# Kernel tuning notes

Measured on AMD Instinct MI355X. Metric: run time of the kernel, lower is better.

The kernel has to match this reference:

```python
import jax, jax.numpy as jnp
import numpy as np

B, N, D = 16, 2048, 64

def setup_inputs() -> dict:
    key = jax.random.key(0)
    kq, kk, kv = jax.random.split(key, 3)
    queries = jax.random.normal(kq, (B, N, D), dtype=jnp.float32)
    keys = jax.random.normal(kk, (B, N, D), dtype=jnp.float32)
    values = jax.random.normal(kv, (B, N, D), dtype=jnp.float32)
    scaling_factor = jnp.asarray(np.sqrt(D), dtype=jnp.float32)
    return {"queries": queries, "keys": keys, "values": values, "scaling_factor": scaling_factor}

def reference(queries, keys, values, scaling_factor):
    # scores: [B, N, N] = Q K^T / scale
    scores = jnp.einsum('bqd,bkd->bqk', queries, keys) / scaling_factor
    atn = jax.nn.softmax(scores, axis=2)
    return jnp.einsum('bqk,bkd->bqd', atn, values)
```

## Files before the change

kernel.cpp:

```cpp
#include <hip/hip_runtime.h>
#include <hip/hip_bf16.h>

#define BATCH 16
#define SEQ 2048
#define DIM 64

typedef __attribute__((ext_vector_type(8))) __bf16 bf16x8;
typedef __attribute__((ext_vector_type(8))) unsigned short u16x8;
typedef __attribute__((ext_vector_type(4))) unsigned int u32x4;
typedef __attribute__((ext_vector_type(16))) float f32x16;

#if __has_builtin(__builtin_amdgcn_exp2f)
#define EXP2F(x) __builtin_amdgcn_exp2f(x)
#else
#define EXP2F(x) __expf(0.69314718055994531f * (x))
#endif

__device__ __forceinline__ unsigned short f2bf_hw(float f) {
    __bf16 h = (__bf16)f;
    return __builtin_bit_cast(unsigned short, h);
}

__device__ __forceinline__ unsigned int pk_bf16(float lo, float hi) {
    unsigned int a = f2bf_hw(lo), b = f2bf_hw(hi);
    return a | (b << 16);
}

__device__ __forceinline__ bf16x8 ld_bf8_g(const unsigned short* p) {
    u16x8 u = *(const u16x8*)p;
    return __builtin_bit_cast(bf16x8, u);
}

__global__ __launch_bounds__(256)
void preconvert_kv(const float* __restrict__ K, const float* __restrict__ V,
                   unsigned short* __restrict__ Ks, unsigned short* __restrict__ Vts) {
    const int tid = threadIdx.x;
    if (blockIdx.x < 256) {
        const int b = blockIdx.x >> 4;
        const int t = blockIdx.x & 15;
        const float* src = K + ((size_t)(b * SEQ + t * 128)) * DIM;
        unsigned short* dst = Ks + ((size_t)(b * 16 + t)) * 8192;
        #pragma unroll
        for (int p = 0; p < 4; ++p) {
            const int cid = p * 256 + tid;
            const int key = cid >> 3, g = cid & 7;
            const int d0 = (g >> 1) * 16 + (g & 1) * 8;
            float4 x0 = *(const float4*)(src + key * DIM + d0);
            float4 x1 = *(const float4*)(src + key * DIM + d0 + 4);
            u16x8 o;
            o[0] = f2bf_hw(x0.x); o[1] = f2bf_hw(x0.y); o[2] = f2bf_hw(x0.z); o[3] = f2bf_hw(x0.w);
            o[4] = f2bf_hw(x1.x); o[5] = f2bf_hw(x1.y); o[6] = f2bf_hw(x1.z); o[7] = f2bf_hw(x1.w);
            *(u16x8*)(dst + (g * 128 + key) * 8) = o;
        }
    } else {
        const int vb = blockIdx.x - 256;
        const int b = vb >> 4;
        const int t = vb & 15;
        const float* src = V + ((size_t)(b * SEQ + t * 128)) * DIM;
        unsigned short* dst = Vts + ((size_t)(b * 16 + t)) * 8192;
        #pragma unroll
        for (int p = 0; p < 4; ++p) {
            const int cid = p * 256 + tid;
            const int g = cid >> 6, d = cid & 63;
            const int k0 = (g >> 1) * 16 + (g & 1) * 8;
            u16x8 o;
            #pragma unroll
            for (int j = 0; j < 8; ++j) o[j] = f2bf_hw(src[(k0 + j) * DIM + d]);
            *(u16x8*)(dst + (g * 64 + d) * 8) = o;
        }
    }
}

__global__ __launch_bounds__(256, 2)
void attn_flash_kernel(const float* __restrict__ Q,
                       const unsigned short* __restrict__ Ks,
                       const unsigned short* __restrict__ Vts,
                       const float* __restrict__ scaling,
                       float* __restrict__ O) {
    __shared__ float comb[3 * 64 * 66];

    const int tid  = threadIdx.x;
    const int w    = tid >> 6;
    const int lane = tid & 63;
    const int m    = lane & 31;
    const int h    = lane >> 5;

    const int x  = blockIdx.x;
    const int b  = ((x & 7) << 1) | ((x >> 3) & 1);
    const int q0 = (x >> 4) * 64;

    const float csc = 1.4426950408889634f / scaling[0];

    bf16x8 aq0[4], aq1[4];
    #pragma unroll
    for (int s = 0; s < 2; ++s) {
        const float* qsrc = Q + ((size_t)(b * SEQ + q0 + s * 32 + m)) * DIM + h * 8;
        #pragma unroll
        for (int c = 0; c < 4; ++c) {
            float4 x0 = *(const float4*)(qsrc + c * 16);
            float4 x1 = *(const float4*)(qsrc + c * 16 + 4);
            u32x4 pk;
            pk[0] = pk_bf16(x0.x * csc, x0.y * csc);
            pk[1] = pk_bf16(x0.z * csc, x0.w * csc);
            pk[2] = pk_bf16(x1.x * csc, x1.y * csc);
            pk[3] = pk_bf16(x1.z * csc, x1.w * csc);
            (s ? aq1 : aq0)[c] = __builtin_bit_cast(bf16x8, pk);
        }
    }

    f32x16 Oacc0[2], Oacc1[2];
    #pragma unroll
    for (int dt = 0; dt < 2; ++dt)
        #pragma unroll
        for (int r = 0; r < 16; ++r) { Oacc0[dt][r] = 0.f; Oacc1[dt][r] = 0.f; }
    float psum0 = 0.f, psum1 = 0.f;

    const unsigned short* Kbase = Ks + ((size_t)(b * 16 + w * 4)) * 8192;
    const unsigned short* Vbase = Vts + ((size_t)(b * 16 + w * 4)) * 8192;

    bf16x8 kc[4], bv[2][2];
    #pragma unroll
    for (int c = 0; c < 4; ++c)
        kc[c] = ld_bf8_g(&Kbase[((c * 2 + h) * 128 + m) * 8]);
    #pragma unroll
    for (int c2 = 0; c2 < 2; ++c2)
        #pragma unroll
        for (int dt = 0; dt < 2; ++dt)
            bv[c2][dt] = ld_bf8_g(&Vbase[((c2 * 2 + h) * 64 + dt * 32 + m) * 8]);

    #pragma unroll 1
    for (int st = 0; st < 16; ++st) {
        f32x16 S0, S1;
        #pragma unroll
        for (int r = 0; r < 16; ++r) { S0[r] = 0.f; S1[r] = 0.f; }
        #pragma unroll
        for (int c = 0; c < 4; ++c) {
            S0 = __builtin_amdgcn_mfma_f32_32x32x16_bf16(kc[c], aq0[c], S0, 0, 0, 0);
            S1 = __builtin_amdgcn_mfma_f32_32x32x16_bf16(kc[c], aq1[c], S1, 0, 0, 0);
        }

        const int stn = (st < 15) ? st + 1 : 15;
        const unsigned short* Ktn = Kbase + (size_t)(stn >> 2) * 8192;
        const unsigned short* Vtn = Vbase + (size_t)(stn >> 2) * 8192;
        const int tn = stn & 3;
        bf16x8 kn[4], vn[2][2];
        #pragma unroll
        for (int c = 0; c < 4; ++c)
            kn[c] = ld_bf8_g(&Ktn[((c * 2 + h) * 128 + tn * 32 + m) * 8]);
        #pragma unroll
        for (int c2 = 0; c2 < 2; ++c2)
            #pragma unroll
            for (int dt = 0; dt < 2; ++dt)
                vn[c2][dt] = ld_bf8_g(&Vtn[(((2 * tn + c2) * 2 + h) * 64 + dt * 32 + m) * 8]);

        unsigned int d0a[8], d0b[8], dsa[8], dsb[8];
        #pragma unroll
        for (int k = 0; k < 4; ++k) {
            float a0 = EXP2F(S0[4 * k + 0]), a1 = EXP2F(S0[4 * k + 1]);
            float a2 = EXP2F(S0[4 * k + 2]), a3 = EXP2F(S0[4 * k + 3]);
            psum0 += (a0 + a1) + (a2 + a3);
            d0a[2 * k + 0] = pk_bf16(a0, a1);
            d0a[2 * k + 1] = pk_bf16(a2, a3);
            float b0 = EXP2F(S1[4 * k + 0]), b1 = EXP2F(S1[4 * k + 1]);
            float b2 = EXP2F(S1[4 * k + 2]), b3 = EXP2F(S1[4 * k + 3]);
            psum1 += (b0 + b1) + (b2 + b3);
            d0b[2 * k + 0] = pk_bf16(b0, b1);
            d0b[2 * k + 1] = pk_bf16(b2, b3);
        }
        #pragma unroll
        for (int i = 0; i < 8; ++i) {
            dsa[i] = (unsigned int)__shfl_xor((int)d0a[i], 32);
            dsb[i] = (unsigned int)__shfl_xor((int)d0b[i], 32);
        }
        #pragma unroll
        for (int c2 = 0; c2 < 2; ++c2) {
            u32x4 bw0, bw1;
            bw0[0] = h ? dsa[4 * c2 + 2] : d0a[4 * c2 + 0];
            bw0[1] = h ? dsa[4 * c2 + 3] : d0a[4 * c2 + 1];
            bw0[2] = h ? d0a[4 * c2 + 2] : dsa[4 * c2 + 0];
            bw0[3] = h ? d0a[4 * c2 + 3] : dsa[4 * c2 + 1];
            bw1[0] = h ? dsb[4 * c2 + 2] : d0b[4 * c2 + 0];
            bw1[1] = h ? dsb[4 * c2 + 3] : d0b[4 * c2 + 1];
            bw1[2] = h ? d0b[4 * c2 + 2] : dsb[4 * c2 + 0];
            bw1[3] = h ? d0b[4 * c2 + 3] : dsb[4 * c2 + 1];
            bf16x8 pb0 = __builtin_bit_cast(bf16x8, bw0);
            bf16x8 pb1 = __builtin_bit_cast(bf16x8, bw1);
            #pragma unroll
            for (int dt = 0; dt < 2; ++dt) {
                Oacc0[dt] = __builtin_amdgcn_mfma_f32_32x32x16_bf16(bv[c2][dt], pb0, Oacc0[dt], 0, 0, 0);
                Oacc1[dt] = __builtin_amdgcn_mfma_f32_32x32x16_bf16(bv[c2][dt], pb1, Oacc1[dt], 0, 0, 0);
            }
        }

        #pragma unroll
        for (int c = 0; c < 4; ++c) kc[c] = kn[c];
        #pragma unroll
        for (int c2 = 0; c2 < 2; ++c2)
            #pragma unroll
            for (int dt = 0; dt < 2; ++dt) bv[c2][dt] = vn[c2][dt];
    }

    float l0 = psum0 + __shfl_xor(psum0, 32);
    float l1 = psum1 + __shfl_xor(psum1, 32);
    if (w > 0) {
        float* dst = comb + ((w - 1) * 64 + lane) * 66;
        #pragma unroll
        for (int dt = 0; dt < 2; ++dt)
            #pragma unroll
            for (int r = 0; r < 16; ++r) {
                dst[dt * 16 + r]      = Oacc0[dt][r];
                dst[33 + dt * 16 + r] = Oacc1[dt][r];
            }
        dst[32] = l0;
        dst[65] = l1;
    }
    __syncthreads();
    if (w == 0) {
        const float* p0 = comb + (0 * 64 + lane) * 66;
        const float* p1 = comb + (1 * 64 + lane) * 66;
        const float* p2 = comb + (2 * 64 + lane) * 66;
        const float invl0 = 1.0f / (l0 + p0[32] + p1[32] + p2[32]);
        const float invl1 = 1.0f / (l1 + p0[65] + p1[65] + p2[65]);
        float* orow0 = O + ((size_t)(b * SEQ + q0 + m)) * DIM;
        float* orow1 = O + ((size_t)(b * SEQ + q0 + 32 + m)) * DIM;
        #pragma unroll
        for (int dt = 0; dt < 2; ++dt) {
            #pragma unroll
            for (int k = 0; k < 4; ++k) {
                float4 o4;
                #pragma unroll
                for (int j = 0; j < 4; ++j) {
                    const int r = 4 * k + j;
                    ((float*)&o4)[j] = (Oacc0[dt][r] + p0[dt * 16 + r] + p1[dt * 16 + r]
                                        + p2[dt * 16 + r]) * invl0;
                }
                *(float4*)(orow0 + dt * 32 + 8 * k + 4 * h) = o4;
                #pragma unroll
                for (int j = 0; j < 4; ++j) {
                    const int r = 4 * k + j;
                    ((float*)&o4)[j] = (Oacc1[dt][r] + p0[33 + dt * 16 + r] + p1[33 + dt * 16 + r]
                                        + p2[33 + dt * 16 + r]) * invl1;
                }
                *(float4*)(orow1 + dt * 32 + 8 * k + 4 * h) = o4;
            }
        }
    }
}

extern "C" void kernel_launch(void* const* d_in, const int* in_sizes, int n_in,
                              void* d_out, int out_size, void* d_ws, size_t ws_size,
                              hipStream_t stream) {
    const float* Q = (const float*)d_in[0];
    const float* K = (const float*)d_in[1];
    const float* V = (const float*)d_in[2];
    const float* scaling = (const float*)d_in[3];
    float* O = (float*)d_out;

    unsigned short* Ks  = (unsigned short*)d_ws;
    unsigned short* Vts = Ks + (size_t)BATCH * 16 * 8192;

    preconvert_kv<<<dim3(512), dim3(256), 0, stream>>>(K, V, Ks, Vts);
    attn_flash_kernel<<<dim3(BATCH * (SEQ / 64)), dim3(256), 0, stream>>>(Q, Ks, Vts, scaling, O);
}
```

Baseline: 106.9 us.

## Permute K key order at preconversion to remove cross-lane shuffles in P@V

The K preconversion now writes keys in a permuted slot order (bits 2 and 3 of the key index swapped within each 32-key group). With that order, the MFMA score accumulator layout already matches the B-operand layout the P@V MFMA expects, so the per-lane exponentials can be packed straight into bf16 operands. This removes the 16 cross-half-wave shuffles and select logic per tile. Correctness depends on the permutation exactly matching the accumulator-to-operand mapping, and the softmax sum is order-independent.

```diff
diff --git a/kernel.cpp b/kernel.cpp
--- a/kernel.cpp
+++ b/kernel.cpp
@@ -43,14 +43,16 @@
         #pragma unroll
         for (int p = 0; p < 4; ++p) {
             const int cid = p * 256 + tid;
-            const int key = cid >> 3, g = cid & 7;
+            const int slot = cid >> 3, g = cid & 7;
+            const int s32 = slot & 31;
+            const int skey = (slot & ~31) | (s32 & ~12) | (((s32 >> 2) & 1) << 3) | (((s32 >> 3) & 1) << 2);
             const int d0 = (g >> 1) * 16 + (g & 1) * 8;
-            float4 x0 = *(const float4*)(src + key * DIM + d0);
-            float4 x1 = *(const float4*)(src + key * DIM + d0 + 4);
+            float4 x0 = *(const float4*)(src + skey * DIM + d0);
+            float4 x1 = *(const float4*)(src + skey * DIM + d0 + 4);
             u16x8 o;
             o[0] = f2bf_hw(x0.x); o[1] = f2bf_hw(x0.y); o[2] = f2bf_hw(x0.z); o[3] = f2bf_hw(x0.w);
             o[4] = f2bf_hw(x1.x); o[5] = f2bf_hw(x1.y); o[6] = f2bf_hw(x1.z); o[7] = f2bf_hw(x1.w);
-            *(u16x8*)(dst + (g * 128 + key) * 8) = o;
+            *(u16x8*)(dst + (g * 128 + slot) * 8) = o;
         }
     } else {
         const int vb = blockIdx.x - 256;
@@ -153,38 +155,22 @@
             for (int dt = 0; dt < 2; ++dt)
                 vn[c2][dt] = ld_bf8_g(&Vtn[(((2 * tn + c2) * 2 + h) * 64 + dt * 32 + m) * 8]);
 
-        unsigned int d0a[8], d0b[8], dsa[8], dsb[8];
-        #pragma unroll
-        for (int k = 0; k < 4; ++k) {
-            float a0 = EXP2F(S0[4 * k + 0]), a1 = EXP2F(S0[4 * k + 1]);
-            float a2 = EXP2F(S0[4 * k + 2]), a3 = EXP2F(S0[4 * k + 3]);
-            psum0 += (a0 + a1) + (a2 + a3);
-            d0a[2 * k + 0] = pk_bf16(a0, a1);
-            d0a[2 * k + 1] = pk_bf16(a2, a3);
-            float b0 = EXP2F(S1[4 * k + 0]), b1 = EXP2F(S1[4 * k + 1]);
-            float b2 = EXP2F(S1[4 * k + 2]), b3 = EXP2F(S1[4 * k + 3]);
-            psum1 += (b0 + b1) + (b2 + b3);
-            d0b[2 * k + 0] = pk_bf16(b0, b1);
-            d0b[2 * k + 1] = pk_bf16(b2, b3);
-        }
-        #pragma unroll
-        for (int i = 0; i < 8; ++i) {
-            dsa[i] = (unsigned int)__shfl_xor((int)d0a[i], 32);
-            dsb[i] = (unsigned int)__shfl_xor((int)d0b[i], 32);
-        }
         #pragma unroll
         for (int c2 = 0; c2 < 2; ++c2) {
-            u32x4 bw0, bw1;
-            bw0[0] = h ? dsa[4 * c2 + 2] : d0a[4 * c2 + 0];
-            bw0[1] = h ? dsa[4 * c2 + 3] : d0a[4 * c2 + 1];
-            bw0[2] = h ? d0a[4 * c2 + 2] : dsa[4 * c2 + 0];
-            bw0[3] = h ? d0a[4 * c2 + 3] : dsa[4 * c2 + 1];
-            bw1[0] = h ? dsb[4 * c2 + 2] : d0b[4 * c2 + 0];
-            bw1[1] = h ? dsb[4 * c2 + 3] : d0b[4 * c2 + 1];
-            bw1[2] = h ? d0b[4 * c2 + 2] : dsb[4 * c2 + 0];
-            bw1[3] = h ? d0b[4 * c2 + 3] : dsb[4 * c2 + 1];
-            bf16x8 pb0 = __builtin_bit_cast(bf16x8, bw0);
-            bf16x8 pb1 = __builtin_bit_cast(bf16x8, bw1);
+            u32x4 pw0, pw1;
+            #pragma unroll
+            for (int i = 0; i < 4; ++i) {
+                float a0 = EXP2F(S0[8 * c2 + 2 * i + 0]);
+                float a1 = EXP2F(S0[8 * c2 + 2 * i + 1]);
+                psum0 += a0 + a1;
+                pw0[i] = pk_bf16(a0, a1);
+                float b0 = EXP2F(S1[8 * c2 + 2 * i + 0]);
+                float b1 = EXP2F(S1[8 * c2 + 2 * i + 1]);
+                psum1 += b0 + b1;
+                pw1[i] = pk_bf16(b0, b1);
+            }
+            bf16x8 pb0 = __builtin_bit_cast(bf16x8, pw0);
+            bf16x8 pb1 = __builtin_bit_cast(bf16x8, pw1);
             #pragma unroll
             for (int dt = 0; dt < 2; ++dt) {
                 Oacc0[dt] = __builtin_amdgcn_mfma_f32_32x32x16_bf16(bv[c2][dt], pb0, Oacc0[dt], 0, 0, 0);
```

Result: slower. 113.2 us (+5.8%).
